# Optimization experiments

Hardware: AMD Instinct MI355X
Metric: run time of the kernel (lower is better)

The kernel has to match this reference:

```python
import jax, jax.numpy as jnp
import numpy as np

M = 8192   # output rows
N = 8192   # input dim
K = 8192   # non_zero_rows (inner dim after dropping empty B rows)
NNZ_A = 256  # nonzeros per row of A (m x k)
NNZ_B = 256  # nonzeros per row of B (k x n)
BATCH = 32


def setup_inputs() -> dict:
    key = jax.random.key(0)
    k1, k2, k3, k4, k5 = jax.random.split(key, 5)
    x = jax.random.normal(k1, (N, BATCH), dtype=jnp.float32)
    a_idx = jax.random.randint(k2, (M, NNZ_A), 0, K, dtype=jnp.int32)
    a_vals = jax.random.normal(k3, (M, NNZ_A), dtype=jnp.float32) * 0.05
    b_idx = jax.random.randint(k4, (K, NNZ_B), 0, N, dtype=jnp.int32)
    b_vals = jax.random.normal(k5, (K, NNZ_B), dtype=jnp.float32) * 0.05
    return {"x": x, "a_idx": a_idx, "a_vals": a_vals, "b_idx": b_idx, "b_vals": b_vals}


def reference(x, a_idx, a_vals, b_idx, b_vals):
    # Double-sparse matvec: y = A @ (B @ x), sparse matrices in ELL form
    # (row-wise column indices + values, equivalent math to the CSR kernel).
    # B @ x: gather x rows per nonzero of B, contract over nnz axis.
    bx = jnp.einsum('kj,kjb->kb', b_vals, x[b_idx])        # [K, BATCH]
    # A @ bx: gather bx rows per nonzero of A.
    y = jnp.einsum('mj,mjb->mb', a_vals, bx[a_idx])        # [M, BATCH]
    # Match torch output layout: (1, batch, m)
    return y.T[None]
```

## Files before the change

kernel.cpp:

```cpp
#include <hip/hip_runtime.h>


#define DIM_M 8192
#define NNZ   256
#define BATCH 32

template <bool TRANSPOSED_OUT>
__global__ __launch_bounds__(256) void ell_spmv(
    const int*   __restrict__ idx,
    const float* __restrict__ vals,
    const float* __restrict__ src,
    float*       __restrict__ dst,
    int rows)
{
    const int wave = threadIdx.x >> 6;
    const int lane = threadIdx.x & 63;
    const int r    = blockIdx.x * 4 + wave;
    const int b    = lane & 31;
    const int h    = lane >> 5;

    const float4* v4 = (const float4*)(vals + (size_t)r * NNZ);
    const int4*   i4 = (const int4*)(idx  + (size_t)r * NNZ);

    float acc = 0.f;
    #pragma unroll 4
    for (int g = 0; g < NNZ / 4; g += 2) {
        const float4 v = v4[g + h];
        const int4   i = i4[g + h];
        acc += v.x * src[(size_t)i.x * BATCH + b];
        acc += v.y * src[(size_t)i.y * BATCH + b];
        acc += v.z * src[(size_t)i.z * BATCH + b];
        acc += v.w * src[(size_t)i.w * BATCH + b];
    }
    acc += __shfl_xor(acc, 32);

    if (h == 0) {
        if (TRANSPOSED_OUT)
            dst[(size_t)b * rows + r] = acc;
        else
            dst[(size_t)r * BATCH + b] = acc;
    }
}

extern "C" void kernel_launch(void* const* d_in, const int* in_sizes, int n_in,
                              void* d_out, int out_size, void* d_ws, size_t ws_size,
                              hipStream_t stream) {
    const float* x      = (const float*)d_in[0];
    const int*   a_idx  = (const int*)  d_in[1];
    const float* a_vals = (const float*)d_in[2];
    const int*   b_idx  = (const int*)  d_in[3];
    const float* b_vals = (const float*)d_in[4];
    float*       out    = (float*)d_out;
    float*       bx     = (float*)d_ws;

    const int rows = DIM_M;
    dim3 block(256);
    dim3 grid(rows / 4);

    ell_spmv<false><<<grid, block, 0, stream>>>(b_idx, b_vals, x,  bx,  rows);
    ell_spmv<true ><<<grid, block, 0, stream>>>(a_idx, a_vals, bx, out, rows);
}
```

Before: 132.5 us.

## Remap ELL SpMV lanes to gather float4 batch slices per nonzero

Changes the thread mapping so each lane handles one nonzero index and four batch columns, gathering 16-byte float4 slices of the source row instead of scalar loads. Index and value loads become nontemporal scalar loads, and partial sums are reduced across 8 nonzero groups with xor shuffles. The transposed output goes through a small shared-memory tile so the stores are more grouped, which adds a block barrier. Each gathered row is now fetched as wider vector loads, at the cost of more shuffle reductions and uncoalesced per-lane index loads.

```diff
diff --git a/kernel.cpp b/kernel.cpp
--- a/kernel.cpp
+++ b/kernel.cpp
@@ -1,44 +1,61 @@
 #include <hip/hip_runtime.h>
 
 
-#define DIM_M 8192
-#define NNZ   256
-#define BATCH 32
+#define NNZ    256
+#define BATCH  32
+#define ROWS   8192
 
 template <bool TRANSPOSED_OUT>
-__global__ __launch_bounds__(256) void ell_spmv(
+__global__ __launch_bounds__(256) void ell_spmv4(
     const int*   __restrict__ idx,
     const float* __restrict__ vals,
     const float* __restrict__ src,
-    float*       __restrict__ dst,
-    int rows)
+    float*       __restrict__ dst)
 {
+    __shared__ float tile[4][BATCH];
+
     const int wave = threadIdx.x >> 6;
     const int lane = threadIdx.x & 63;
     const int r    = blockIdx.x * 4 + wave;
-    const int b    = lane & 31;
-    const int h    = lane >> 5;
+    const int s    = lane & 7;
+    const int q    = lane >> 3;
 
-    const float4* v4 = (const float4*)(vals + (size_t)r * NNZ);
-    const int4*   i4 = (const int4*)(idx  + (size_t)r * NNZ);
+    const int rowoff = r * NNZ;
+    float4 acc = {0.f, 0.f, 0.f, 0.f};
 
-    float acc = 0.f;
     #pragma unroll 4
-    for (int g = 0; g < NNZ / 4; g += 2) {
-        const float4 v = v4[g + h];
-        const int4   i = i4[g + h];
-        acc += v.x * src[(size_t)i.x * BATCH + b];
-        acc += v.y * src[(size_t)i.y * BATCH + b];
-        acc += v.z * src[(size_t)i.z * BATCH + b];
-        acc += v.w * src[(size_t)i.w * BATCH + b];
+    for (int g = 0; g < NNZ / 8; ++g) {
+        const int   j  = rowoff + g * 8 + q;
+        const int   ix = __builtin_nontemporal_load(idx + j);
+        const float v  = __builtin_nontemporal_load(vals + j);
+        const float4 xv = *(const float4*)(src + ix * BATCH + s * 4);
+        acc.x += v * xv.x;
+        acc.y += v * xv.y;
+        acc.z += v * xv.z;
+        acc.w += v * xv.w;
     }
-    acc += __shfl_xor(acc, 32);
 
-    if (h == 0) {
-        if (TRANSPOSED_OUT)
-            dst[(size_t)b * rows + r] = acc;
-        else
-            dst[(size_t)r * BATCH + b] = acc;
+    #pragma unroll
+    for (int d = 8; d < 64; d <<= 1) {
+        acc.x += __shfl_xor(acc.x, d);
+        acc.y += __shfl_xor(acc.y, d);
+        acc.z += __shfl_xor(acc.z, d);
+        acc.w += __shfl_xor(acc.w, d);
+    }
+
+    if (!TRANSPOSED_OUT) {
+        if (q == 0)
+            *(float4*)(dst + r * BATCH + s * 4) = acc;
+    } else {
+        if (q == 0)
+            *(float4*)(&tile[wave][s * 4]) = acc;
+        __syncthreads();
+        const int t = threadIdx.x;
+        if (t < 4 * BATCH) {
+            const int b  = t >> 2;
+            const int rr = t & 3;
+            dst[b * ROWS + blockIdx.x * 4 + rr] = tile[rr][b];
+        }
     }
 }
 
@@ -53,10 +70,9 @@
     float*       out    = (float*)d_out;
     float*       bx     = (float*)d_ws;
 
-    const int rows = DIM_M;
     dim3 block(256);
-    dim3 grid(rows / 4);
+    dim3 grid(ROWS / 4);
 
-    ell_spmv<false><<<grid, block, 0, stream>>>(b_idx, b_vals, x,  bx,  rows);
-    ell_spmv<true ><<<grid, block, 0, stream>>>(a_idx, a_vals, bx, out, rows);
+    ell_spmv4<false><<<grid, block, 0, stream>>>(b_idx, b_vals, x,  bx);
+    ell_spmv4<true ><<<grid, block, 0, stream>>>(a_idx, a_vals, bx, out);
 }
```

Measured after the change: 122.3 us. -7.7%, faster.
